# Kernel optimization log

Hardware: AMD Instinct MI355X
Metric: run time of the kernel (lower is better)

The kernel has to match this reference:

```python
import jax, jax.numpy as jnp
import numpy as np

N, E, ELG = 5000, 50000, 200000      # nodes, edges of g, edges of line graph
NDIM, EDIM, H, L = 512, 512, 8, 2    # hidden sizes, heads, layers
DK = NDIM // H
REL = 128                            # number of relation types
SCALE = float(np.sqrt(DK))


def _ln(x, g, b, eps=1e-5):
    m = x.mean(-1, keepdims=True)
    v = ((x - m) ** 2).mean(-1, keepdims=True)
    return (x - m) * jax.lax.rsqrt(v + eps) * g + b


def _ffn(x, W1, b1, W2, b2, g, b):
    # FFN with residual + layernorm (post-LN transformer FFN)
    return _ln(x + jnp.maximum(x @ W1 + b1, 0.0) @ W2 + b2, g, b)


def _attend(q, k, v, e, src, dst, n_seg):
    # q,k,v: [n_seg, H, DK]; e: optional per-edge feature [Ne, H, DK]
    ks = k[src] if e is None else k[src] + e
    vs = v[src] if e is None else v[src] + e
    # scaled_exp: exp(clamp(score / sqrt(dk), -10, 10))
    score = jnp.exp(jnp.clip((ks * q[dst]).sum(-1) / SCALE, -10.0, 10.0))  # [Ne, H]
    wv = jax.ops.segment_sum(vs * score[..., None], dst, num_segments=n_seg)
    z = jax.ops.segment_sum(score, dst, num_segments=n_seg)
    return wv / z[..., None]  # div_by_z


def setup_inputs() -> dict:
    key = jax.random.key(0)
    keys = iter(jax.random.split(key, 80))
    nxt = lambda: next(keys)

    def nrm(shape, s=0.02):
        return jax.random.normal(nxt(), shape, dtype=jnp.float32) * s

    inp = {}
    inp['x'] = jax.random.normal(nxt(), (N, NDIM), dtype=jnp.float32)
    inp['edge_feat'] = jax.random.randint(nxt(), (E,), 0, REL, dtype=jnp.int32)
    inp['src_ids'] = jax.random.randint(nxt(), (E,), 0, N, dtype=jnp.int32)
    # cover every node / every lg-node so softmax denominators are nonzero
    inp['dst_ids'] = jnp.concatenate([jnp.arange(N, dtype=jnp.int32),
                                      jax.random.randint(nxt(), (E - N,), 0, N, dtype=jnp.int32)])
    inp['lg_src'] = jax.random.randint(nxt(), (ELG,), 0, E, dtype=jnp.int32)
    inp['lg_dst'] = jnp.concatenate([jnp.arange(E, dtype=jnp.int32),
                                     jax.random.randint(nxt(), (ELG - E,), 0, E, dtype=jnp.int32)])
    inp['rel_embed'] = nrm((REL, EDIM), 1.0)
    for p in ['n', 'e']:
        din = NDIM if p == 'n' else EDIM
        inp[p + '_Wq'] = nrm((L, din, NDIM)); inp[p + '_bq'] = jnp.zeros((L, NDIM), jnp.float32)
        inp[p + '_Wk'] = nrm((L, din, NDIM)); inp[p + '_Wv'] = nrm((L, din, NDIM))
        inp[p + '_Wo'] = nrm((L, NDIM, din)); inp[p + '_bo'] = jnp.zeros((L, din), jnp.float32)
        inp[p + '_ln_g'] = jnp.ones((L, din), jnp.float32); inp[p + '_ln_b'] = jnp.zeros((L, din), jnp.float32)
        inp[p + '_f1'] = nrm((L, din, 4 * din)); inp[p + '_fb1'] = jnp.zeros((L, 4 * din), jnp.float32)
        inp[p + '_f2'] = nrm((L, 4 * din, din)); inp[p + '_fb2'] = jnp.zeros((L, din), jnp.float32)
        inp[p + '_fln_g'] = jnp.ones((L, din), jnp.float32); inp[p + '_fln_b'] = jnp.zeros((L, din), jnp.float32)
    return inp


def reference(x, edge_feat, src_ids, dst_ids, lg_src, lg_dst, rel_embed,
              n_Wq, n_bq, n_Wk, n_Wv, n_Wo, n_bo, n_ln_g, n_ln_b,
              n_f1, n_fb1, n_f2, n_fb2, n_fln_g, n_fln_b,
              e_Wq, e_bq, e_Wk, e_Wv, e_Wo, e_bo, e_ln_g, e_ln_b,
              e_f1, e_fb1, e_f2, e_fb2, e_fln_g, e_fln_b):
    lg_x = rel_embed[edge_feat]  # [E, EDIM]
    for i in range(L):
        # ---- node update on g (attention over incoming edges, edge feats added to k,v) ----
        q = (x @ n_Wq[i] + n_bq[i]).reshape(N, H, DK)
        k = (x @ n_Wk[i]).reshape(N, H, DK)
        v = (x @ n_Wv[i]).reshape(N, H, DK)
        e = lg_x.reshape(E, H, DK)  # edim == ndim (relation_share_heads=False)
        o = _attend(q, k, v, e, src_ids, dst_ids, N).reshape(N, NDIM)
        out_x = _ln(x + o @ n_Wo[i] + n_bo[i], n_ln_g[i], n_ln_b[i])
        out_x = _ffn(out_x, n_f1[i], n_fb1[i], n_f2[i], n_fb2[i], n_fln_g[i], n_fln_b[i])
        # ---- edge update on line graph (uses PRE-update node feats; q+=dst, k+=src, v+=src) ----
        src_x = x[src_ids]
        dst_x = x[dst_ids]
        qe = (lg_x @ e_Wq[i] + e_bq[i] + dst_x).reshape(E, H, DK)
        ke = (lg_x @ e_Wk[i] + src_x).reshape(E, H, DK)
        ve = (lg_x @ e_Wv[i] + src_x).reshape(E, H, DK)
        oe = _attend(qe, ke, ve, None, lg_src, lg_dst, E).reshape(E, NDIM)
        out_lg = _ln(lg_x + oe @ e_Wo[i] + e_bo[i], e_ln_g[i], e_ln_b[i])
        out_lg = _ffn(out_lg, e_f1[i], e_fb1[i], e_f2[i], e_fb2[i], e_fln_g[i], e_fln_b[i])
        x, lg_x = out_x, out_lg
    return (x, lg_x)
```

## Files before the change

kernel.cpp:

```cpp
#include <hip/hip_runtime.h>
#include <math.h>

#define NNODES 5000
#define NEDGES 50000
#define NELG   200000
#define DMODEL 512
#define NH     8
#define NLAYERS 2

typedef __bf16 bf16x8 __attribute__((ext_vector_type(8)));
typedef float  f32x4  __attribute__((ext_vector_type(4)));
typedef unsigned short us8v __attribute__((ext_vector_type(8)));
typedef unsigned short us4v __attribute__((ext_vector_type(4)));

__device__ __forceinline__ float b2f(unsigned short u) {
    union { unsigned int i; float f; } c;
    c.i = ((unsigned int)u) << 16;
    return c.f;
}
__device__ __forceinline__ unsigned short f2b(float f) {
    union { float f; unsigned int i; } c;
    c.f = f;
    unsigned int i = c.i;
    return (unsigned short)((i + 0x7fffu + ((i >> 16) & 1u)) >> 16);
}

struct GemmDst {
    unsigned short* C0; unsigned short* C1; unsigned short* C2;
    const unsigned short* a0; const unsigned short* a1; const unsigned short* a2;
    const int* x0; const int* x1; const int* x2;
    const float* b0; const float* b1; const float* b2;
};

#define BM 128
#define BN 128
#define BK 32

__global__ __launch_bounds__(256) void mfma_gemm_kernel(
    const unsigned short* __restrict__ A, const unsigned short* __restrict__ Bt,
    GemmDst P, int M, int K, int N, int secN, int relu)
{
    __shared__ __align__(16) unsigned short ldsA[BM * BK];
    __shared__ __align__(16) unsigned short ldsB[BN * BK];

    const int nbx  = gridDim.x;
    const int nb   = nbx * gridDim.y;
    const int wgid = blockIdx.y * nbx + blockIdx.x;
    const int xcd  = wgid & 7;
    const int ii   = wgid >> 3;
    const int q8   = nb >> 3, r8 = nb & 7;
    const int base = (xcd < r8) ? xcd * (q8 + 1) : r8 * (q8 + 1) + (xcd - r8) * q8;
    const int tl   = base + ii;
    const int rowBase = (tl / nbx) * BM;
    const int colBase = (tl % nbx) * BN;

    const int tid  = threadIdx.x;
    const int lane = tid & 63;
    const int wave = tid >> 6;
    const int quad = lane >> 4;
    const int l16  = lane & 15;
    const int wm = (wave >> 1) * 64;
    const int wn = (wave & 1) * 64;

    const int g0 = tid, g1 = tid + 256;
    const int r0 = g0 >> 2, r1 = g1 >> 2;
    const int c0g = (g0 & 3) ^ ((r0 >> 1) & 3);
    const int c1g = (g1 & 3) ^ ((r1 >> 1) & 3);
    int ra0 = rowBase + r0; if (ra0 > M - 1) ra0 = M - 1;
    int ra1 = rowBase + r1; if (ra1 > M - 1) ra1 = M - 1;
    const unsigned short* gA0 = A + (size_t)ra0 * K + c0g * 8;
    const unsigned short* gA1 = A + (size_t)ra1 * K + c1g * 8;
    const unsigned short* gB0 = Bt + (size_t)(colBase + r0) * K + c0g * 8;
    const unsigned short* gB1 = Bt + (size_t)(colBase + r1) * K + c1g * 8;
    unsigned short* lA0 = ldsA + g0 * 8;
    unsigned short* lA1 = ldsA + g1 * 8;
    unsigned short* lB0 = ldsB + g0 * 8;
    unsigned short* lB1 = ldsB + g1 * 8;

    const int swz = (l16 >> 1) & 3;
    const int ca = (quad ^ swz) * 8;

    const f32x4 zv = {0.f, 0.f, 0.f, 0.f};
    f32x4 acc[4][4];
    #pragma unroll
    for (int i = 0; i < 4; ++i)
        #pragma unroll
        for (int j = 0; j < 4; ++j) acc[i][j] = zv;

    for (int k0 = 0; k0 < K; k0 += BK) {
        __builtin_amdgcn_global_load_lds(
            (const __attribute__((address_space(1))) void*)(gA0 + k0),
            (__attribute__((address_space(3))) void*)lA0, 16, 0, 0);
        __builtin_amdgcn_global_load_lds(
            (const __attribute__((address_space(1))) void*)(gA1 + k0),
            (__attribute__((address_space(3))) void*)lA1, 16, 0, 0);
        __builtin_amdgcn_global_load_lds(
            (const __attribute__((address_space(1))) void*)(gB0 + k0),
            (__attribute__((address_space(3))) void*)lB0, 16, 0, 0);
        __builtin_amdgcn_global_load_lds(
            (const __attribute__((address_space(1))) void*)(gB1 + k0),
            (__attribute__((address_space(3))) void*)lB1, 16, 0, 0);
        __syncthreads();

        bf16x8 af[4], bfr[4];
        #pragma unroll
        for (int i = 0; i < 4; ++i)
            af[i] = *(const bf16x8*)(ldsA + (wm + i * 16 + l16) * BK + ca);
        #pragma unroll
        for (int j = 0; j < 4; ++j)
            bfr[j] = *(const bf16x8*)(ldsB + (wn + j * 16 + l16) * BK + ca);
        #pragma unroll
        for (int i = 0; i < 4; ++i)
            #pragma unroll
            for (int j = 0; j < 4; ++j)
                acc[i][j] = __builtin_amdgcn_mfma_f32_16x16x32_bf16(
                    bfr[j], af[i], acc[i][j], 0, 0, 0);
        __syncthreads();
    }

    const int sec   = colBase / secN;
    const int cbase = colBase - sec * secN;
    unsigned short*       Cs = (sec == 0) ? P.C0 : ((sec == 1) ? P.C1 : P.C2);
    const unsigned short* ad = (sec == 0) ? P.a0 : ((sec == 1) ? P.a1 : P.a2);
    const int*            gx = (sec == 0) ? P.x0 : ((sec == 1) ? P.x1 : P.x2);
    const float*          bs = (sec == 0) ? P.b0 : ((sec == 1) ? P.b1 : P.b2);

    f32x4 b4[4];
    #pragma unroll
    for (int j = 0; j < 4; ++j) {
        const int n0 = cbase + wn + j * 16 + quad * 4;
        b4[j] = bs ? *(const f32x4*)(bs + n0) : zv;
    }

    #pragma unroll
    for (int i = 0; i < 4; ++i) {
        const int row = rowBase + wm + i * 16 + l16;
        if (row >= M) continue;
        const int arow = gx ? gx[row] : row;
        const unsigned short* ar = ad ? ad + (size_t)arow * secN : nullptr;
        unsigned short* crow = Cs + (size_t)row * secN;
        #pragma unroll
        for (int j = 0; j < 4; ++j) {
            const int n0 = cbase + wn + j * 16 + quad * 4;
            f32x4 v = acc[i][j];
            v += b4[j];
            if (ar) {
                const us4v r4 = *(const us4v*)(ar + n0);
                #pragma unroll
                for (int r = 0; r < 4; ++r) v[r] += b2f(r4[r]);
            }
            if (relu) {
                #pragma unroll
                for (int r = 0; r < 4; ++r) v[r] = fmaxf(v[r], 0.0f);
            }
            us4v o4;
            #pragma unroll
            for (int r = 0; r < 4; ++r) o4[r] = f2b(v[r]);
            *(us4v*)(crow + n0) = o4;
        }
    }
}

#define TM 256
#define TN 256
#define TK 64

__global__ __launch_bounds__(512, 1) void mfma_gemm256_kernel(
    const unsigned short* __restrict__ A, const unsigned short* __restrict__ Bt,
    GemmDst P, int M, int K, int N, int secN, int relu)
{
    __shared__ __align__(16) unsigned short ldsA[2][TM * TK];
    __shared__ __align__(16) unsigned short ldsB[2][TN * TK];

    const int nbx  = gridDim.x;
    const int nb   = nbx * gridDim.y;
    const int wgid = blockIdx.y * nbx + blockIdx.x;
    const int xcd  = wgid & 7;
    const int ii   = wgid >> 3;
    const int q8   = nb >> 3, r8 = nb & 7;
    const int base = (xcd < r8) ? xcd * (q8 + 1) : r8 * (q8 + 1) + (xcd - r8) * q8;
    const int tl   = base + ii;
    const int rowBase = (tl / nbx) * TM;
    const int colBase = (tl % nbx) * TN;

    const int tid  = threadIdx.x;
    const int lane = tid & 63;
    const int wave = tid >> 6;
    const int quad = lane >> 4;
    const int l16  = lane & 15;
    const int wr   = wave >> 2;
    const int wc   = wave & 3;

    const unsigned short* srcA[4];
    const unsigned short* srcB[4];
    int ldsOff[4];
    #pragma unroll
    for (int j = 0; j < 4; ++j) {
        const int p = j * 512 + tid;
        const int r = p >> 3;
        const int c = (p & 7) ^ (r & 7);
        ldsOff[j] = p * 8;
        int rA = rowBase + r; if (rA > M - 1) rA = M - 1;
        srcA[j] = A + (size_t)rA * K + c * 8;
        srcB[j] = Bt + (size_t)(colBase + r) * K + c * 8;
    }

    const int ca0 = (quad       ^ (l16 & 7)) * 8;
    const int ca1 = ((quad + 4) ^ (l16 & 7)) * 8;
    const int aRow0 = wr * 128 + l16;
    const int bRow0 = wc * 64 + l16;

    const f32x4 zv = {0.f, 0.f, 0.f, 0.f};
    f32x4 acc[8][4];
    #pragma unroll
    for (int i = 0; i < 8; ++i)
        #pragma unroll
        for (int j = 0; j < 4; ++j) acc[i][j] = zv;

#define STAGE256(buf, t)                                                      \
    {                                                                         \
        unsigned short* dA = ldsA[buf];                                       \
        unsigned short* dB = ldsB[buf];                                       \
        const int ko = (t) * TK;                                              \
        _Pragma("unroll")                                                     \
        for (int j = 0; j < 4; ++j)                                           \
            __builtin_amdgcn_global_load_lds(                                 \
                (const __attribute__((address_space(1))) void*)(srcA[j] + ko),\
                (__attribute__((address_space(3))) void*)(dA + ldsOff[j]),    \
                16, 0, 0);                                                    \
        _Pragma("unroll")                                                     \
        for (int j = 0; j < 4; ++j)                                           \
            __builtin_amdgcn_global_load_lds(                                 \
                (const __attribute__((address_space(1))) void*)(srcB[j] + ko),\
                (__attribute__((address_space(3))) void*)(dB + ldsOff[j]),    \
                16, 0, 0);                                                    \
    }

#define COMPUTE256(buf)                                                       \
    {                                                                         \
        const unsigned short* bA = ldsA[buf];                                 \
        const unsigned short* bB = ldsB[buf];                                 \
        _Pragma("unroll")                                                     \
        for (int ks = 0; ks < 2; ++ks) {                                      \
            const int cs = ks ? ca1 : ca0;                                    \
            bf16x8 afr[8], bfr[4];                                            \
            _Pragma("unroll")                                                 \
            for (int m = 0; m < 8; ++m)                                       \
                afr[m] = *(const bf16x8*)(bA + (aRow0 + m * 16) * TK + cs);   \
            _Pragma("unroll")                                                 \
            for (int n = 0; n < 4; ++n)                                       \
                bfr[n] = *(const bf16x8*)(bB + (bRow0 + n * 16) * TK + cs);   \
            _Pragma("unroll")                                                 \
            for (int m = 0; m < 8; ++m)                                       \
                _Pragma("unroll")                                             \
                for (int n = 0; n < 4; ++n)                                   \
                    acc[m][n] = __builtin_amdgcn_mfma_f32_16x16x32_bf16(      \
                        bfr[n], afr[m], acc[m][n], 0, 0, 0);                  \
        }                                                                     \
    }

    const int nt = K / TK;

    STAGE256(0, 0);
    STAGE256(1, 1);
    asm volatile("s_waitcnt vmcnt(8)" ::: "memory");
    __builtin_amdgcn_s_barrier();
    __builtin_amdgcn_sched_barrier(0);

    for (int t = 0; t < nt - 2; ++t) {
        COMPUTE256(t & 1);
        __builtin_amdgcn_sched_barrier(0);
        __builtin_amdgcn_s_barrier();
        STAGE256(t & 1, t + 2);
        asm volatile("s_waitcnt vmcnt(8)" ::: "memory");
        __builtin_amdgcn_s_barrier();
        __builtin_amdgcn_sched_barrier(0);
    }
    COMPUTE256(nt & 1);
    __builtin_amdgcn_sched_barrier(0);
    asm volatile("s_waitcnt vmcnt(0)" ::: "memory");
    __builtin_amdgcn_s_barrier();
    __builtin_amdgcn_sched_barrier(0);
    COMPUTE256((nt - 1) & 1);

#undef STAGE256
#undef COMPUTE256

    const int sec   = colBase / secN;
    const int cbase = colBase - sec * secN;
    unsigned short*       Cs = (sec == 0) ? P.C0 : ((sec == 1) ? P.C1 : P.C2);
    const unsigned short* ad = (sec == 0) ? P.a0 : ((sec == 1) ? P.a1 : P.a2);
    const int*            gx = (sec == 0) ? P.x0 : ((sec == 1) ? P.x1 : P.x2);
    const float*          bs = (sec == 0) ? P.b0 : ((sec == 1) ? P.b1 : P.b2);

    f32x4 b4[4];
    #pragma unroll
    for (int n = 0; n < 4; ++n) {
        const int n0 = cbase + wc * 64 + n * 16 + quad * 4;
        b4[n] = bs ? *(const f32x4*)(bs + n0) : zv;
    }

    #pragma unroll
    for (int m = 0; m < 8; ++m) {
        const int row = rowBase + wr * 128 + m * 16 + l16;
        if (row >= M) continue;
        const int arow = gx ? gx[row] : row;
        const unsigned short* ar = ad ? ad + (size_t)arow * secN : nullptr;
        unsigned short* crow = Cs + (size_t)row * secN;
        #pragma unroll
        for (int n = 0; n < 4; ++n) {
            const int n0 = cbase + wc * 64 + n * 16 + quad * 4;
            f32x4 v = acc[m][n];
            v += b4[n];
            if (ar) {
                const us4v r4 = *(const us4v*)(ar + n0);
                #pragma unroll
                for (int r = 0; r < 4; ++r) v[r] += b2f(r4[r]);
            }
            if (relu) {
                #pragma unroll
                for (int r = 0; r < 4; ++r) v[r] = fmaxf(v[r], 0.0f);
            }
            us4v o4;
            #pragma unroll
            for (int r = 0; r < 4; ++r) o4[r] = f2b(v[r]);
            *(us4v*)(crow + n0) = o4;
        }
    }
}

__global__ __launch_bounds__(256) void transpose_cast_kernel(
    const float* __restrict__ W, unsigned short* __restrict__ Wt, int K, int N)
{
    __shared__ float t[32][33];
    const int n0 = blockIdx.x << 5, k0 = blockIdx.y << 5;
    const int tx = threadIdx.x & 31, ty = threadIdx.x >> 5;
    #pragma unroll
    for (int r = 0; r < 32; r += 8)
        t[ty + r][tx] = W[(size_t)(k0 + ty + r) * N + n0 + tx];
    __syncthreads();
    #pragma unroll
    for (int r = 0; r < 32; r += 8)
        Wt[(size_t)(n0 + ty + r) * K + k0 + tx] = f2b(t[tx][ty + r]);
}

__global__ __launch_bounds__(256) void ln_kernel(
    unsigned short* __restrict__ x, const float* __restrict__ g,
    const float* __restrict__ b, int M)
{
    const int row = blockIdx.x * 4 + (threadIdx.x >> 6);
    if (row >= M) return;
    const int lane = threadIdx.x & 63;
    unsigned short* xr = x + (size_t)row * DMODEL;

    float vals[8];
    float s = 0.f, s2 = 0.f;
    #pragma unroll
    for (int i = 0; i < 8; ++i) {
        const float v = b2f(xr[lane + i * 64]);
        vals[i] = v; s += v; s2 += v * v;
    }
    #pragma unroll
    for (int o = 32; o > 0; o >>= 1) {
        s  += __shfl_down(s, o);
        s2 += __shfl_down(s2, o);
    }
    s  = __shfl(s, 0);
    s2 = __shfl(s2, 0);
    const float m = s * (1.0f / DMODEL);
    const float var = s2 * (1.0f / DMODEL) - m * m;
    const float r = rsqrtf(var + 1e-5f);
    #pragma unroll
    for (int i = 0; i < 8; ++i) {
        const int c = lane + i * 64;
        xr[c] = f2b((vals[i] - m) * r * g[c] + b[c]);
    }
}

__global__ __launch_bounds__(256) void hist_kernel(
    const int* __restrict__ dst, int* __restrict__ cnt, int ne)
{
    const int j = blockIdx.x * 256 + threadIdx.x;
    if (j < ne) atomicAdd(&cnt[dst[j]], 1);
}

__global__ __launch_bounds__(1024) void scan_kernel(
    const int* __restrict__ cnt, int* __restrict__ off,
    int* __restrict__ cur, int n)
{
    __shared__ int part[1024];
    const int t = threadIdx.x;
    const int chunk = (n + 1023) >> 10;
    const int lo = t * chunk;
    int hi = lo + chunk; if (hi > n) hi = n;
    int s = 0;
    for (int i = lo; i < hi; ++i) s += cnt[i];
    part[t] = s;
    __syncthreads();
    #pragma unroll
    for (int o = 1; o < 1024; o <<= 1) {
        int v = (t >= o) ? part[t - o] : 0;
        __syncthreads();
        part[t] += v;
        __syncthreads();
    }
    int base = (t == 0) ? 0 : part[t - 1];
    const int total = part[1023];
    for (int i = lo; i < hi; ++i) {
        const int c = cnt[i];
        off[i] = base; cur[i] = base;
        base += c;
    }
    if (t == 1023) off[n] = total;
}

__global__ __launch_bounds__(256) void scatter_kernel(
    const int* __restrict__ dst, int* __restrict__ cur,
    int* __restrict__ idx, int ne)
{
    const int j = blockIdx.x * 256 + threadIdx.x;
    if (j < ne) {
        const int p = atomicAdd(&cur[dst[j]], 1);
        idx[p] = j;
    }
}

__global__ __launch_bounds__(256) void attend_kernel(
    unsigned short* __restrict__ q,
    const unsigned short* __restrict__ k,
    const unsigned short* __restrict__ v,
    const unsigned short* __restrict__ efeat,
    const int* __restrict__ src,
    const int* __restrict__ off, const int* __restrict__ idx,
    int nseg)
{
    const int wave = threadIdx.x >> 6, lane = threadIdx.x & 63;
    const int seg = blockIdx.x * 4 + wave;
    if (seg >= nseg) return;
    const int c8 = lane * 8;
    unsigned short* qrow = q + (size_t)seg * DMODEL;

    const us8v q8 = *(const us8v*)(qrow + c8);
    float qv[8];
    #pragma unroll
    for (int j = 0; j < 8; ++j) qv[j] = b2f(q8[j]);

    float acc[8] = {0.f, 0.f, 0.f, 0.f, 0.f, 0.f, 0.f, 0.f};
    float zsum = 0.f;
    const int lo = off[seg], hi = off[seg + 1];
    for (int jj = lo; jj < hi; ++jj) {
        const int e = idx[jj];
        const int s = src[e];
        const us8v k8 = *(const us8v*)(k + (size_t)s * DMODEL + c8);
        const us8v v8 = *(const us8v*)(v + (size_t)s * DMODEL + c8);
        float p = 0.f;
        float vv[8];
        if (efeat) {
            const us8v e8 = *(const us8v*)(efeat + (size_t)e * DMODEL + c8);
            #pragma unroll
            for (int j = 0; j < 8; ++j) {
                const float ef = b2f(e8[j]);
                p = fmaf(b2f(k8[j]) + ef, qv[j], p);
                vv[j] = b2f(v8[j]) + ef;
            }
        } else {
            #pragma unroll
            for (int j = 0; j < 8; ++j) {
                p = fmaf(b2f(k8[j]), qv[j], p);
                vv[j] = b2f(v8[j]);
            }
        }
        p += __shfl_xor(p, 1);
        p += __shfl_xor(p, 2);
        p += __shfl_xor(p, 4);
        float sc = p * 0.125f;
        sc = fminf(fmaxf(sc, -10.0f), 10.0f);
        sc = __expf(sc);
        zsum += sc;
        #pragma unroll
        for (int j = 0; j < 8; ++j) acc[j] = fmaf(sc, vv[j], acc[j]);
    }

    const float rz = 1.0f / zsum;
    us8v o8;
    #pragma unroll
    for (int j = 0; j < 8; ++j) o8[j] = f2b(acc[j] * rz);
    *(us8v*)(qrow + c8) = o8;
}

__global__ __launch_bounds__(256) void gather_rel_kernel(
    const float* __restrict__ rel, const int* __restrict__ ef,
    unsigned short* __restrict__ lg)
{
    const int idx = blockIdx.x * 256 + threadIdx.x;
    if (idx >= NEDGES * DMODEL) return;
    const int e = idx >> 9;
    const int col = idx & 511;
    lg[idx] = f2b(rel[(size_t)ef[e] * DMODEL + col]);
}

__global__ __launch_bounds__(256) void cast_f2b_kernel(
    const float* __restrict__ in, unsigned short* __restrict__ out, int n)
{
    const int idx = blockIdx.x * 256 + threadIdx.x;
    if (idx < n) out[idx] = f2b(in[idx]);
}

__global__ __launch_bounds__(256) void cast_b2f_kernel(
    const unsigned short* __restrict__ in, float* __restrict__ out, int n)
{
    const int idx = blockIdx.x * 256 + threadIdx.x;
    if (idx < n) out[idx] = b2f(in[idx]);
}

__global__ __launch_bounds__(256) void zero_kernel(float4* __restrict__ p, int n4)
{
    const int idx = blockIdx.x * 256 + threadIdx.x;
    if (idx < n4) p[idx] = make_float4(0.f, 0.f, 0.f, 0.f);
}

static inline void mgemm(hipStream_t st, const unsigned short* A, const unsigned short* Bt,
                         const float* bias, const unsigned short* add, const int* gidx,
                         unsigned short* C, int M, int K, int N, int relu)
{
    GemmDst P = {C, nullptr, nullptr, add, nullptr, nullptr,
                 gidx, nullptr, nullptr, bias, nullptr, nullptr};
    dim3 g(N / BN, (M + BM - 1) / BM);
    mfma_gemm_kernel<<<g, 256, 0, st>>>(A, Bt, P, M, K, N, N, relu);
}

static inline void mgemm256(hipStream_t st, const unsigned short* A, const unsigned short* Bt,
                            const float* bias, const unsigned short* add, const int* gidx,
                            unsigned short* C, int M, int K, int N, int relu)
{
    GemmDst P = {C, nullptr, nullptr, add, nullptr, nullptr,
                 gidx, nullptr, nullptr, bias, nullptr, nullptr};
    dim3 g(N / TN, (M + TM - 1) / TM);
    mfma_gemm256_kernel<<<g, 512, 0, st>>>(A, Bt, P, M, K, N, N, relu);
}

static inline void mgemm_qkv(hipStream_t st, const unsigned short* A, const unsigned short* Bt,
                             const float* biasQ,
                             const unsigned short* addQ, const int* gxQ,
                             const unsigned short* addKV, const int* gxKV,
                             unsigned short* Cq, unsigned short* Ck, unsigned short* Cv,
                             int M, int K)
{
    GemmDst P = {Cq, Ck, Cv, addQ, addKV, addKV,
                 gxQ, gxKV, gxKV, biasQ, nullptr, nullptr};
    dim3 g(1536 / BN, (M + BM - 1) / BM);
    mfma_gemm_kernel<<<g, 256, 0, st>>>(A, Bt, P, M, K, 1536, 512, 0);
}

static inline void mgemm256_qkv(hipStream_t st, const unsigned short* A, const unsigned short* Bt,
                                const float* biasQ,
                                const unsigned short* addQ, const int* gxQ,
                                const unsigned short* addKV, const int* gxKV,
                                unsigned short* Cq, unsigned short* Ck, unsigned short* Cv,
                                int M, int K)
{
    GemmDst P = {Cq, Ck, Cv, addQ, addKV, addKV,
                 gxQ, gxKV, gxKV, biasQ, nullptr, nullptr};
    dim3 g(1536 / TN, (M + TM - 1) / TM);
    mfma_gemm256_kernel<<<g, 512, 0, st>>>(A, Bt, P, M, K, 1536, 512, 0);
}

static inline void tcast(hipStream_t st, const float* W, unsigned short* Wt, int K, int N)
{
    dim3 g(N / 32, K / 32);
    transpose_cast_kernel<<<g, 256, 0, st>>>(W, Wt, K, N);
}
static inline void zero(hipStream_t st, void* p, size_t nfloats)
{
    const int n4 = (int)(nfloats / 4);
    zero_kernel<<<(n4 + 255) / 256, 256, 0, st>>>((float4*)p, n4);
}

extern "C" void kernel_launch(void* const* d_in, const int* in_sizes, int n_in,
                              void* d_out, int out_size, void* d_ws, size_t ws_size,
                              hipStream_t stream)
{
    const float* x_in      = (const float*)d_in[0];
    const int*   edge_feat = (const int*)d_in[1];
    const int*   src_ids   = (const int*)d_in[2];
    const int*   dst_ids   = (const int*)d_in[3];
    const int*   lg_src    = (const int*)d_in[4];
    const int*   lg_dst    = (const int*)d_in[5];
    const float* rel_embed = (const float*)d_in[6];

    const float* n_Wq = (const float*)d_in[7];   const float* n_bq = (const float*)d_in[8];
    const float* n_Wk = (const float*)d_in[9];   const float* n_Wv = (const float*)d_in[10];
    const float* n_Wo = (const float*)d_in[11];  const float* n_bo = (const float*)d_in[12];
    const float* n_lg = (const float*)d_in[13];  const float* n_lb = (const float*)d_in[14];
    const float* n_f1 = (const float*)d_in[15];  const float* n_fb1 = (const float*)d_in[16];
    const float* n_f2 = (const float*)d_in[17];  const float* n_fb2 = (const float*)d_in[18];
    const float* n_fg = (const float*)d_in[19];  const float* n_fb = (const float*)d_in[20];

    const float* e_Wq = (const float*)d_in[21];  const float* e_bq = (const float*)d_in[22];
    const float* e_Wk = (const float*)d_in[23];  const float* e_Wv = (const float*)d_in[24];
    const float* e_Wo = (const float*)d_in[25];  const float* e_bo = (const float*)d_in[26];
    const float* e_lg = (const float*)d_in[27];  const float* e_lb = (const float*)d_in[28];
    const float* e_f1 = (const float*)d_in[29];  const float* e_fb1 = (const float*)d_in[30];
    const float* e_f2 = (const float*)d_in[31];  const float* e_fb2 = (const float*)d_in[32];
    const float* e_fg = (const float*)d_in[33];  const float* e_fb = (const float*)d_in[34];

    const int XSZ  = NNODES * DMODEL;
    const int LGSZ = NEDGES * DMODEL;

    char* ws = (char*)d_ws;
    unsigned short* lg16  = (unsigned short*)(ws);
    unsigned short* ve16  = (unsigned short*)(ws + 51200000);
    int* n_off = (int*)(ws + 102400000);
    int* n_cur = (int*)(ws + 102420480);
    int* n_idx = (int*)(ws + 102440960);
    int* e_off = (int*)(ws + 102641664);
    int* e_cur = (int*)(ws + 102842368);
    int* e_idx = (int*)(ws + 103043072);
    unsigned short* xbufA = (unsigned short*)(ws + 110400000);
    unsigned short* xbufB = (unsigned short*)(ws + 115520000);

    char* ob = (char*)d_out;
    unsigned short* qe16 = (unsigned short*)(ob);
    unsigned short* ke16 = (unsigned short*)(ob + 51200000);
    unsigned short* ehid = (unsigned short*)(ob);
    unsigned short* nq16 = (unsigned short*)(ob);
    unsigned short* nk16 = (unsigned short*)(ob + 5120000);
    unsigned short* nv16 = (unsigned short*)(ob + 10240000);
    unsigned short* nhid = (unsigned short*)(ob);
    unsigned short* wtq  = (unsigned short*)(ob + 102400000);
    unsigned short* wtk  = (unsigned short*)(ob + 102924288);
    unsigned short* wtv  = (unsigned short*)(ob + 103448576);
    unsigned short* wto  = (unsigned short*)(ob + 103972864);
    unsigned short* wtf1 = (unsigned short*)(ob + 104497152);
    unsigned short* wtf2 = (unsigned short*)(ob + 106594304);

    cast_f2b_kernel<<<(XSZ + 255) / 256, 256, 0, stream>>>(x_in, xbufA, XSZ);
    gather_rel_kernel<<<(LGSZ + 255) / 256, 256, 0, stream>>>(rel_embed, edge_feat, lg16);

    zero(stream, n_cur, NNODES);
    zero(stream, e_cur, NEDGES);
    hist_kernel<<<(NEDGES + 255) / 256, 256, 0, stream>>>(dst_ids, n_cur, NEDGES);
    hist_kernel<<<(NELG + 255) / 256, 256, 0, stream>>>(lg_dst, e_cur, NELG);
    scan_kernel<<<1, 1024, 0, stream>>>(n_cur, n_off, n_cur, NNODES);
    scan_kernel<<<1, 1024, 0, stream>>>(e_cur, e_off, e_cur, NEDGES);
    scatter_kernel<<<(NEDGES + 255) / 256, 256, 0, stream>>>(dst_ids, n_cur, n_idx, NEDGES);
    scatter_kernel<<<(NELG + 255) / 256, 256, 0, stream>>>(lg_dst, e_cur, e_idx, NELG);

    unsigned short* xc = xbufA;
    unsigned short* xn = xbufB;

    for (int i = 0; i < NLAYERS; ++i) {
        const size_t wo  = (size_t)i * DMODEL * DMODEL;
        const size_t bo_ = (size_t)i * DMODEL;
        const size_t f1o = (size_t)i * DMODEL * 4 * DMODEL;
        const size_t b1o = (size_t)i * 4 * DMODEL;
        const size_t f2o = (size_t)i * 4 * DMODEL * DMODEL;

        tcast(stream, n_Wq + wo, wtq, 512, 512);
        tcast(stream, n_Wk + wo, wtk, 512, 512);
        tcast(stream, n_Wv + wo, wtv, 512, 512);
        tcast(stream, n_Wo + wo, wto, 512, 512);
        tcast(stream, n_f1 + f1o, wtf1, 512, 2048);
        tcast(stream, n_f2 + f2o, wtf2, 2048, 512);

        mgemm_qkv(stream, xc, wtq, n_bq + bo_,
                  nullptr, nullptr, nullptr, nullptr,
                  nq16, nk16, nv16, NNODES, 512);

        attend_kernel<<<(NNODES + 3) / 4, 256, 0, stream>>>(
            nq16, nk16, nv16, lg16, src_ids, n_off, n_idx, NNODES);

        mgemm(stream, nq16, wto, n_bo + bo_, xc, nullptr, xn, NNODES, 512, 512, 0);
        ln_kernel<<<(NNODES + 3) / 4, 256, 0, stream>>>(xn, n_lg + bo_, n_lb + bo_, NNODES);
        mgemm(stream, xn, wtf1, n_fb1 + b1o, nullptr, nullptr, nhid, NNODES, 512, 2048, 1);
        mgemm(stream, nhid, wtf2, n_fb2 + bo_, xn, nullptr, xn, NNODES, 2048, 512, 0);
        ln_kernel<<<(NNODES + 3) / 4, 256, 0, stream>>>(xn, n_fg + bo_, n_fb + bo_, NNODES);

        tcast(stream, e_Wq + wo, wtq, 512, 512);
        tcast(stream, e_Wk + wo, wtk, 512, 512);
        tcast(stream, e_Wv + wo, wtv, 512, 512);
        tcast(stream, e_Wo + wo, wto, 512, 512);

        mgemm256_qkv(stream, lg16, wtq, e_bq + bo_,
                     xc, dst_ids, xc, src_ids,
                     qe16, ke16, ve16, NEDGES, 512);

        attend_kernel<<<(NEDGES + 3) / 4, 256, 0, stream>>>(
            qe16, ke16, ve16, nullptr, lg_src, e_off, e_idx, NEDGES);

        mgemm(stream, qe16, wto, e_bo + bo_, lg16, nullptr, lg16, NEDGES, 512, 512, 0);
        ln_kernel<<<(NEDGES + 3) / 4, 256, 0, stream>>>(lg16, e_lg + bo_, e_lb + bo_, NEDGES);

        tcast(stream, e_f1 + f1o, wtf1, 512, 2048);
        tcast(stream, e_f2 + f2o, wtf2, 2048, 512);
        for (int c = 0; c < 2; ++c) {
            unsigned short* y1c = lg16 + (size_t)c * 25000 * DMODEL;
            mgemm256(stream, y1c, wtf1, e_fb1 + b1o, nullptr, nullptr, ehid, 25000, 512, 2048, 1);
            mgemm(stream, ehid, wtf2, e_fb2 + bo_, y1c, nullptr, y1c, 25000, 2048, 512, 0);
        }
        ln_kernel<<<(NEDGES + 3) / 4, 256, 0, stream>>>(lg16, e_fg + bo_, e_fb + bo_, NEDGES);

        unsigned short* t = xc; xc = xn; xn = t;
    }

    float* out_f = (float*)d_out;
    cast_b2f_kernel<<<(XSZ + 255) / 256, 256, 0, stream>>>(xc, out_f, XSZ);
    cast_b2f_kernel<<<(LGSZ + 255) / 256, 256, 0, stream>>>(lg16, out_f + XSZ, LGSZ);
}
```

Measured before the change: 2.270 ms.

## Restructure GEMM main loop into four interleaved phases with staggered prefetch

Replaces the two-stage compute/stage loop of the 256-wide GEMM with a per-k-tile loop split into four phases. Each phase loads half the A fragments from LDS, issues part of the next tile's global-to-LDS copies, then runs its MFMAs at raised wave priority via s_setprio. The aim is to spread memory issue across the compute and lower register pressure by holding 4 A fragments instead of 8. In exchange it adds many more workgroup barriers per tile and a full vmcnt(0) wait at the end of every tile, which can expose load latency.

```diff
diff --git a/kernel.cpp b/kernel.cpp
--- a/kernel.cpp
+++ b/kernel.cpp
@@ -217,74 +217,72 @@
         #pragma unroll
         for (int j = 0; j < 4; ++j) acc[i][j] = zv;
 
-#define STAGE256(buf, t)                                                      \
+#define STG2(dst, src, kn, j0)                                                \
     {                                                                         \
-        unsigned short* dA = ldsA[buf];                                       \
-        unsigned short* dB = ldsB[buf];                                       \
-        const int ko = (t) * TK;                                              \
         _Pragma("unroll")                                                     \
-        for (int j = 0; j < 4; ++j)                                           \
+        for (int j = (j0); j < (j0) + 2; ++j)                                 \
             __builtin_amdgcn_global_load_lds(                                 \
-                (const __attribute__((address_space(1))) void*)(srcA[j] + ko),\
-                (__attribute__((address_space(3))) void*)(dA + ldsOff[j]),    \
+                (const __attribute__((address_space(1))) void*)((src)[j] + (kn)), \
+                (__attribute__((address_space(3))) void*)((dst) + ldsOff[j]), \
                 16, 0, 0);                                                    \
+    }
+
+#define PHASE(CS, MBASE, READB, STG)                                          \
+    {                                                                         \
         _Pragma("unroll")                                                     \
-        for (int j = 0; j < 4; ++j)                                           \
-            __builtin_amdgcn_global_load_lds(                                 \
-                (const __attribute__((address_space(1))) void*)(srcB[j] + ko),\
-                (__attribute__((address_space(3))) void*)(dB + ldsOff[j]),    \
-                16, 0, 0);                                                    \
-    }
-
-#define COMPUTE256(buf)                                                       \
-    {                                                                         \
-        const unsigned short* bA = ldsA[buf];                                 \
-        const unsigned short* bB = ldsB[buf];                                 \
-        _Pragma("unroll")                                                     \
-        for (int ks = 0; ks < 2; ++ks) {                                      \
-            const int cs = ks ? ca1 : ca0;                                    \
-            bf16x8 afr[8], bfr[4];                                            \
-            _Pragma("unroll")                                                 \
-            for (int m = 0; m < 8; ++m)                                       \
-                afr[m] = *(const bf16x8*)(bA + (aRow0 + m * 16) * TK + cs);   \
+        for (int m = 0; m < 4; ++m)                                           \
+            afr[m] = *(const bf16x8*)(bA + (aRow0 + ((MBASE) + m) * 16) * TK + (CS)); \
+        if (READB) {                                                          \
             _Pragma("unroll")                                                 \
             for (int n = 0; n < 4; ++n)                                       \
-                bfr[n] = *(const bf16x8*)(bB + (bRow0 + n * 16) * TK + cs);   \
+                bfr[n] = *(const bf16x8*)(bB + (bRow0 + n * 16) * TK + (CS)); \
+        }                                                                     \
+        STG;                                                                  \
+        __builtin_amdgcn_s_barrier();                                         \
+        __builtin_amdgcn_sched_barrier(0);                                    \
+        __builtin_amdgcn_s_setprio(1);                                        \
+        _Pragma("unroll")                                                     \
+        for (int m = 0; m < 4; ++m)                                           \
             _Pragma("unroll")                                                 \
-            for (int m = 0; m < 8; ++m)                                       \
-                _Pragma("unroll")                                             \
-                for (int n = 0; n < 4; ++n)                                   \
-                    acc[m][n] = __builtin_amdgcn_mfma_f32_16x16x32_bf16(      \
-                        bfr[n], afr[m], acc[m][n], 0, 0, 0);                  \
-        }                                                                     \
+            for (int n = 0; n < 4; ++n)                                       \
+                acc[(MBASE) + m][n] = __builtin_amdgcn_mfma_f32_16x16x32_bf16(\
+                    bfr[n], afr[m], acc[(MBASE) + m][n], 0, 0, 0);            \
+        __builtin_amdgcn_s_setprio(0);                                        \
+        __builtin_amdgcn_sched_barrier(0);                                    \
     }
 
     const int nt = K / TK;
 
-    STAGE256(0, 0);
-    STAGE256(1, 1);
-    asm volatile("s_waitcnt vmcnt(8)" ::: "memory");
-    __builtin_amdgcn_s_barrier();
-    __builtin_amdgcn_sched_barrier(0);
-
-    for (int t = 0; t < nt - 2; ++t) {
-        COMPUTE256(t & 1);
-        __builtin_amdgcn_sched_barrier(0);
-        __builtin_amdgcn_s_barrier();
-        STAGE256(t & 1, t + 2);
-        asm volatile("s_waitcnt vmcnt(8)" ::: "memory");
-        __builtin_amdgcn_s_barrier();
-        __builtin_amdgcn_sched_barrier(0);
-    }
-    COMPUTE256(nt & 1);
-    __builtin_amdgcn_sched_barrier(0);
+    STG2(ldsA[0], srcA, 0, 0); STG2(ldsA[0], srcA, 0, 2);
+    STG2(ldsB[0], srcB, 0, 0); STG2(ldsB[0], srcB, 0, 2);
     asm volatile("s_waitcnt vmcnt(0)" ::: "memory");
     __builtin_amdgcn_s_barrier();
     __builtin_amdgcn_sched_barrier(0);
-    COMPUTE256((nt - 1) & 1);
-
-#undef STAGE256
-#undef COMPUTE256
+
+    for (int t = 0; t < nt; ++t) {
+        const int cur = t & 1;
+        const unsigned short* bA = ldsA[cur];
+        const unsigned short* bB = ldsB[cur];
+        unsigned short* dA = ldsA[cur ^ 1];
+        unsigned short* dB = ldsB[cur ^ 1];
+        const bool pf = (t + 1 < nt);
+        const int kn = (t + 1) * TK;
+        bf16x8 afr[4], bfr[4];
+
+        PHASE(ca0, 0, 1, if (pf) STG2(dA, srcA, kn, 0));
+        __builtin_amdgcn_s_barrier();
+        PHASE(ca0, 4, 0, if (pf) STG2(dA, srcA, kn, 2));
+        __builtin_amdgcn_s_barrier();
+        PHASE(ca1, 0, 1, if (pf) STG2(dB, srcB, kn, 0));
+        __builtin_amdgcn_s_barrier();
+        PHASE(ca1, 4, 0, if (pf) STG2(dB, srcB, kn, 2));
+        if (pf) asm volatile("s_waitcnt vmcnt(0)" ::: "memory");
+        __builtin_amdgcn_s_barrier();
+        __builtin_amdgcn_sched_barrier(0);
+    }
+
+#undef PHASE
+#undef STG2
 
     const int sec   = colBase / secN;
     const int cbase = colBase - sec * secN;
```

Result: no change. 2.259 ms (-0.5%).
